# Kernel optimization log

Measured on AMD Instinct MI355X. Metric: run time of the kernel, lower is better.

The kernel has to match this reference:

```python
import jax, jax.numpy as jnp
import numpy as np

B, D, H, K = 4096, 768, 16384, 32


def setup_inputs() -> dict:
    key = jax.random.key(0)
    k1, k2, k3 = jax.random.split(key, 3)
    return {
        "x": jax.random.normal(k1, (B, D), dtype=jnp.float32),
        "W_enc": jax.random.normal(k2, (H, D), dtype=jnp.float32) * 0.02,
        "b_enc": jnp.zeros((H,), dtype=jnp.float32),
        "W_dec": jax.random.normal(k3, (D, H), dtype=jnp.float32) * 0.02,
        "b_dec": jnp.zeros((D,), dtype=jnp.float32),
        "k": K,
    }


def reference(x, W_enc, b_enc, W_dec, b_dec, k):
    # Encode: z = ReLU(x W_enc^T + b_enc)   -> [B, H]
    z = jax.nn.relu(jnp.einsum("bd,hd->bh", x, W_enc) + b_enc)
    # Top-k mask along hidden dim (k < H)
    _, topk_idx = jax.lax.top_k(z, k)                      # [B, k]
    rows = jnp.arange(z.shape[0])[:, None]                 # [B, 1]
    mask = jnp.zeros_like(z).at[rows, topk_idx].set(1.0)   # scatter ones
    z = z * mask
    # Decode: x_hat = z W_dec^T + b_dec     -> [B, D]
    x_hat = jnp.einsum("bh,dh->bd", z, W_dec) + b_dec
    return (x_hat, z)
```

## Files before the change

### kernel.cpp

```cpp
#include <hip/hip_runtime.h>

constexpr int NB = 4096;
constexpr int ND = 768;
constexpr int NH = 16384;
constexpr int NK = 32;
constexpr int CAND_MAX = 512;
#define DELTA 0.04f

typedef __bf16 bf16x8 __attribute__((ext_vector_type(8)));
typedef float  f32x4  __attribute__((ext_vector_type(4)));

constexpr size_t OFF_XBF   = 0;
constexpr size_t OFF_WENCB = OFF_XBF   + (size_t)NB * ND * 2;
constexpr size_t OFF_WDECT = OFF_WENCB + (size_t)NH * ND * 2;
constexpr size_t OFF_CIDX  = OFF_WDECT + (size_t)NH * ND * 4;
constexpr size_t OFF_CCNT  = OFF_CIDX  + (size_t)NB * CAND_MAX * 4;
constexpr size_t OFF_ZA    = OFF_CCNT  + (size_t)NB * 4;
constexpr size_t ZA_BYTES  = (size_t)NB * NH * 2;

__device__ inline unsigned short f2bf(float f) {
  unsigned u = __float_as_uint(f);
  unsigned r = u + 0x7fffu + ((u >> 16) & 1u);
  return (unsigned short)(r >> 16);
}

__device__ __forceinline__ void gld_lds16(const unsigned short* g, unsigned short* s) {
  __builtin_amdgcn_global_load_lds((const __attribute__((address_space(1))) void*)g,
                                   (__attribute__((address_space(3))) void*)s, 16, 0, 0);
}

__global__ __launch_bounds__(256) void cast_bf16_kernel(const float* __restrict__ in,
                                                        unsigned short* __restrict__ out,
                                                        int n4) {
  int stride = gridDim.x * 256;
  for (int i = blockIdx.x * 256 + threadIdx.x; i < n4; i += stride) {
    float4 v = ((const float4*)in)[i];
    unsigned long long p = (unsigned long long)f2bf(v.x)
                         | ((unsigned long long)f2bf(v.y) << 16)
                         | ((unsigned long long)f2bf(v.z) << 32)
                         | ((unsigned long long)f2bf(v.w) << 48);
    ((unsigned long long*)out)[i] = p;
  }
}

__global__ __launch_bounds__(256) void transpose_kernel(const float* __restrict__ in,
                                                        float* __restrict__ out) {
  __shared__ float tile[32][33];
  int hb = blockIdx.x * 32, db = blockIdx.y * 32;
  int tx = threadIdx.x, ty = threadIdx.y;
#pragma unroll
  for (int i = 0; i < 4; ++i)
    tile[ty + i * 8][tx] = in[(size_t)(db + ty + i * 8) * NH + hb + tx];
  __syncthreads();
#pragma unroll
  for (int i = 0; i < 4; ++i)
    out[(size_t)(hb + ty + i * 8) * ND + db + tx] = tile[tx][ty + i * 8];
}

__global__ __launch_bounds__(512) void encode_gemm_kernel(
    const unsigned short* __restrict__ Abf,
    const unsigned short* __restrict__ Bbf,
    const float* __restrict__ b_enc,
    unsigned short* __restrict__ za) {
  __shared__ __align__(16) unsigned short lds_all[3 * 16384];

  int bid = blockIdx.x;
  int xx = bid & 7;
  int jj = bid >> 3;
  int st = jj >> 4;
  int w  = jj & 15;
  int g  = st * 8 + xx;
  int bm = (g & 3) * 4 + (w & 3);
  int bn = (g >> 2) * 4 + (w >> 2);
  int m0 = bm * 256, n0 = bn * 256;

  int tid = threadIdx.x;
  int wid = tid >> 6, l = tid & 63;
  int wr = wid >> 2, wc = wid & 3;
  int lr = l & 15, lk = l >> 4;

#define STAGE_A(nbuf, ktile, t) do {                                              \
    int c_ = (t) * 512 + tid; int r_ = c_ >> 2;                                   \
    int lu_ = (c_ & 3) ^ ((r_ >> 1) & 3);                                         \
    gld_lds16(Abf + (size_t)(m0 + r_) * ND + (ktile) * 32 + lu_ * 8,              \
              lds_all + (nbuf) * 16384 + ((t) * 512 + (wid << 6)) * 8);           \
  } while (0)
#define STAGE_B(nbuf, ktile, t) do {                                              \
    int c_ = (t) * 512 + tid; int r_ = c_ >> 2;                                   \
    int lu_ = (c_ & 3) ^ ((r_ >> 1) & 3);                                         \
    gld_lds16(Bbf + (size_t)(n0 + r_) * ND + (ktile) * 32 + lu_ * 8,              \
              lds_all + (nbuf) * 16384 + 8192 + ((t) * 512 + (wid << 6)) * 8);    \
  } while (0)

  f32x4 acc[8][4] = {};

  STAGE_A(0, 0, 0); STAGE_A(0, 0, 1); STAGE_B(0, 0, 0); STAGE_B(0, 0, 1);
  STAGE_A(1, 1, 0); STAGE_A(1, 1, 1); STAGE_B(1, 1, 0); STAGE_B(1, 1, 1);
  asm volatile("s_waitcnt vmcnt(4)" ::: "memory");
  __builtin_amdgcn_s_barrier();
  __builtin_amdgcn_sched_barrier(0);

  int cur = 0;
  for (int kt = 0; kt < 24; ++kt) {
    int nx = cur + 2; if (nx >= 3) nx -= 3;
    const unsigned short* Ab = lds_all + cur * 16384;
    const unsigned short* Bb = Ab + 8192;
    bf16x8 aF[4], bF[4];

#pragma unroll
    for (int fj = 0; fj < 4; ++fj) {
      int row = wc * 64 + fj * 16 + lr;
      int pu = lk ^ ((row >> 1) & 3);
      bF[fj] = *(const bf16x8*)(Bb + row * 32 + pu * 8);
    }
#pragma unroll
    for (int fi = 0; fi < 4; ++fi) {
      int row = wr * 128 + fi * 16 + lr;
      int pu = lk ^ ((row >> 1) & 3);
      aF[fi] = *(const bf16x8*)(Ab + row * 32 + pu * 8);
    }
    if (kt < 22) { STAGE_A(nx, kt + 2, 0); STAGE_A(nx, kt + 2, 1); }
    __builtin_amdgcn_s_setprio(1);
#pragma unroll
    for (int fi = 0; fi < 4; ++fi)
#pragma unroll
      for (int fj = 0; fj < 4; ++fj)
        acc[fi][fj] = __builtin_amdgcn_mfma_f32_16x16x32_bf16(aF[fi], bF[fj], acc[fi][fj], 0, 0, 0);
    __builtin_amdgcn_s_setprio(0);

#pragma unroll
    for (int fi = 0; fi < 4; ++fi) {
      int row = wr * 128 + (4 + fi) * 16 + lr;
      int pu = lk ^ ((row >> 1) & 3);
      aF[fi] = *(const bf16x8*)(Ab + row * 32 + pu * 8);
    }
    if (kt < 22) { STAGE_B(nx, kt + 2, 0); STAGE_B(nx, kt + 2, 1); }
    __builtin_amdgcn_s_setprio(1);
#pragma unroll
    for (int fi = 0; fi < 4; ++fi)
#pragma unroll
      for (int fj = 0; fj < 4; ++fj)
        acc[4 + fi][fj] = __builtin_amdgcn_mfma_f32_16x16x32_bf16(aF[fi], bF[fj], acc[4 + fi][fj], 0, 0, 0);
    __builtin_amdgcn_s_setprio(0);

    if (kt < 23) {
      if (kt == 22) asm volatile("s_waitcnt vmcnt(0)" ::: "memory");
      else          asm volatile("s_waitcnt vmcnt(4)" ::: "memory");
      __builtin_amdgcn_s_barrier();
      __builtin_amdgcn_sched_barrier(0);
    }
    cur = (cur == 2) ? 0 : cur + 1;
  }
#undef STAGE_A
#undef STAGE_B

  __syncthreads();
  unsigned short* ep = lds_all + wid * 4096;
#pragma unroll
  for (int half = 0; half < 2; ++half) {
#pragma unroll
    for (int fj = 0; fj < 4; ++fj) {
      float bias = b_enc[n0 + wc * 64 + fj * 16 + lr];
#pragma unroll
      for (int i2 = 0; i2 < 4; ++i2) {
#pragma unroll
        for (int q = 0; q < 4; ++q) {
          int row = i2 * 16 + lk * 4 + q;
          int col = fj * 16 + lr;
          float v = fmaxf(acc[half * 4 + i2][fj][q] + bias, 0.0f);
          ep[row * 64 + (((col >> 3) ^ (row & 7)) * 8) + (col & 7)] = f2bf(v);
        }
      }
    }
    __syncthreads();
#pragma unroll
    for (int t = 0; t < 8; ++t) {
      int row = t * 8 + (l >> 3);
      int u = (l & 7) ^ (row & 7);
      int4 d = *(const int4*)&ep[row * 64 + u * 8];
      *(int4*)(za + (size_t)(m0 + wr * 128 + half * 64 + row) * NH
                    + n0 + wc * 64 + (l & 7) * 8) = d;
    }
    __syncthreads();
  }
}


__device__ __forceinline__ float bisect_thr(const uint4* v, int* wcnt, int tid) {
  unsigned lo = 0u, hi = 0x7F80u;
  for (int it = 0; it < 15; ++it) {
    unsigned mid = (lo + hi) >> 1;
    int c = 0;
#pragma unroll
    for (int i = 0; i < 8; ++i) {
      const unsigned* p = (const unsigned*)&v[i];
#pragma unroll
      for (int e = 0; e < 4; ++e) {
        unsigned u = p[e];
        c += ((u & 0xFFFFu) >= mid) ? 1 : 0;
        c += ((u >> 16) >= mid) ? 1 : 0;
      }
    }
#pragma unroll
    for (int off = 32; off; off >>= 1) c += __shfl_xor(c, off, 64);
    if ((tid & 63) == 0) wcnt[tid >> 6] = c;
    __syncthreads();
    int tot = wcnt[0] + wcnt[1] + wcnt[2] + wcnt[3];
    __syncthreads();
    if (tot >= NK) {
      lo = mid;
      if (tot <= 48) break;
    } else {
      hi = mid;
    }
  }
  float thr = __uint_as_float(lo << 16) - DELTA;
  return (thr < 1e-12f) ? 1e-12f : thr;
}

__device__ __forceinline__ void topk_wave0(const float* cv, const int* ci, int cnt,
                                           float* sv, int* si, int l) {
  float lv[8]; int lh[8];
#pragma unroll
  for (int ii = 0; ii < 8; ++ii) {
    int c = l + 64 * ii;
    if (c < cnt) { lv[ii] = cv[c]; lh[ii] = ci[c]; }
    else         { lv[ii] = -1.f;  lh[ii] = 0x7fffffff; }
  }
  for (int r = 0; r < NK; ++r) {
    float bv = -1.f; int bh = 0x7fffffff; int bl = l; int bii = 0;
#pragma unroll
    for (int ii = 0; ii < 8; ++ii)
      if (lv[ii] > bv || (lv[ii] == bv && lh[ii] < bh)) { bv = lv[ii]; bh = lh[ii]; bii = ii; }
#pragma unroll
    for (int off = 32; off; off >>= 1) {
      float ov = __shfl_xor(bv, off, 64);
      int   oh = __shfl_xor(bh, off, 64);
      int   ol = __shfl_xor(bl, off, 64);
      int   oi = __shfl_xor(bii, off, 64);
      if (ov > bv || (ov == bv && oh < bh)) { bv = ov; bh = oh; bl = ol; bii = oi; }
    }
    if (l == 0) {
      if (bv > -0.5f) { sv[r] = bv; si[r] = bh; }
      else            { sv[r] = 0.f; si[r] = -1; }
    }
#pragma unroll
    for (int ii = 0; ii < 8; ++ii)
      if (ii == bii && l == bl && bv > -0.5f) lv[ii] = -1.f;
  }
}

__global__ __launch_bounds__(256) void select_kernel(const unsigned short* __restrict__ za,
                                                     int* __restrict__ cand_idx,
                                                     int* __restrict__ cand_cnt) {
  int b = blockIdx.x, tid = threadIdx.x;
  const uint4* zrow = (const uint4*)(za + (size_t)b * NH);
  uint4 v[8];
#pragma unroll
  for (int i = 0; i < 8; ++i) v[i] = zrow[tid + 256 * i];

  __shared__ int wcnt[4];
  __shared__ int lcnt;
  float thr = bisect_thr(v, wcnt, tid);
  if (tid == 0) lcnt = 0;
  __syncthreads();
#pragma unroll
  for (int i = 0; i < 8; ++i) {
    const unsigned* p = (const unsigned*)&v[i];
#pragma unroll
    for (int e = 0; e < 4; ++e) {
      unsigned u = p[e];
      int hbase = (tid + 256 * i) * 8 + e * 2;
      float f0 = __uint_as_float((u & 0xFFFFu) << 16);
      float f1 = __uint_as_float(u & 0xFFFF0000u);
      if (f0 >= thr) { int s = atomicAdd(&lcnt, 1); if (s < CAND_MAX) cand_idx[(size_t)b * CAND_MAX + s] = hbase; }
      if (f1 >= thr) { int s = atomicAdd(&lcnt, 1); if (s < CAND_MAX) cand_idx[(size_t)b * CAND_MAX + s] = hbase + 1; }
    }
  }
  __syncthreads();
  if (tid == 0) cand_cnt[b] = (lcnt < CAND_MAX) ? lcnt : CAND_MAX;
}

__device__ __forceinline__ void finalize_core(
    int b, int tid, int wid, int l, int cnt,
    const float* __restrict__ W_enc, const float* __restrict__ b_enc,
    const float* __restrict__ WdecT, const float* __restrict__ b_dec,
    const float* xr, float* cv, const int* ci, float* sv, int* si,
    float* __restrict__ zout, float* __restrict__ xhat) {
  const float4* xr4 = (const float4*)xr;
  for (int c = wid; c < cnt; c += 4) {
    int h = ci[c];
    const float4* wrow4 = (const float4*)(W_enc + (size_t)h * ND);
    float4 s4 = make_float4(0.f, 0.f, 0.f, 0.f);
#pragma unroll
    for (int i = 0; i < 3; ++i) {
      float4 wv = wrow4[l + 64 * i];
      float4 xv = xr4[l + 64 * i];
      s4.x = fmaf(wv.x, xv.x, s4.x);
      s4.y = fmaf(wv.y, xv.y, s4.y);
      s4.z = fmaf(wv.z, xv.z, s4.z);
      s4.w = fmaf(wv.w, xv.w, s4.w);
    }
    float s = (s4.x + s4.y) + (s4.z + s4.w);
#pragma unroll
    for (int off = 32; off; off >>= 1) s += __shfl_xor(s, off, 64);
    if (l == 0) cv[c] = fmaxf(s + b_enc[h], 0.f);
  }
  __syncthreads();

  if (wid == 0) {
    topk_wave0(cv, ci, cnt, sv, si, l);
  } else {
    float4 z4 = make_float4(0.f, 0.f, 0.f, 0.f);
    float4* zr = (float4*)(zout + (size_t)b * NH);
    for (int i = tid - 64; i < NH / 4; i += 192) zr[i] = z4;
  }
  __syncthreads();

  if (tid < NK) {
    int s = si[tid];
    if (s >= 0) zout[(size_t)b * NH + s] = sv[tid];
  }

  if (tid < ND / 4) {
    float4 a = ((const float4*)b_dec)[tid];
#pragma unroll 8
    for (int j = 0; j < NK; ++j) {
      int hj = si[j]; hj = (hj < 0) ? 0 : hj;
      float vj = sv[j];
      float4 wv = ((const float4*)(WdecT + (size_t)hj * ND))[tid];
      a.x = fmaf(vj, wv.x, a.x);
      a.y = fmaf(vj, wv.y, a.y);
      a.z = fmaf(vj, wv.z, a.z);
      a.w = fmaf(vj, wv.w, a.w);
    }
    ((float4*)(xhat + (size_t)b * ND))[tid] = a;
  }
}

__global__ __launch_bounds__(256) void finalize_kernel(
    const float* __restrict__ x, const float* __restrict__ W_enc,
    const float* __restrict__ b_enc,
    const int* __restrict__ cand_idx, const int* __restrict__ cand_cnt,
    const float* __restrict__ WdecT, const float* __restrict__ b_dec,
    float* __restrict__ zout, float* __restrict__ xhat) {
  int b = blockIdx.x, tid = threadIdx.x;
  int wid = tid >> 6, l = tid & 63;
  __shared__ __align__(16) float xr[ND];
  __shared__ float cv[CAND_MAX];
  __shared__ int   ci[CAND_MAX];
  __shared__ float sv[NK];
  __shared__ int   si[NK];

  int cnt = cand_cnt[b];
  const float4* xrow = (const float4*)(x + (size_t)b * ND);
  for (int i = tid; i < ND / 4; i += 256) ((float4*)xr)[i] = xrow[i];
  for (int c = tid; c < cnt; c += 256) ci[c] = cand_idx[(size_t)b * CAND_MAX + c];
  __syncthreads();
  finalize_core(b, tid, wid, l, cnt, W_enc, b_enc, WdecT, b_dec,
                xr, cv, ci, sv, si, zout, xhat);
}

__global__ __launch_bounds__(256) void fused_finalize_kernel(
    const unsigned short* __restrict__ za,
    const float* __restrict__ x, const float* __restrict__ W_enc,
    const float* __restrict__ b_enc,
    const float* __restrict__ WdecT, const float* __restrict__ b_dec,
    float* __restrict__ zout, float* __restrict__ xhat) {
  int b = blockIdx.x, tid = threadIdx.x;
  int wid = tid >> 6, l = tid & 63;
  __shared__ __align__(16) float xr[ND];
  __shared__ float cv[CAND_MAX];
  __shared__ int   ci[CAND_MAX];
  __shared__ float sv[NK];
  __shared__ int   si[NK];
  __shared__ int   wcnt[4];
  __shared__ int   lcnt;

  const uint4* zrow = (const uint4*)(za + (size_t)b * NH);
  uint4 v[8];
#pragma unroll
  for (int i = 0; i < 8; ++i) v[i] = zrow[tid + 256 * i];
  const float4* xrow = (const float4*)(x + (size_t)b * ND);
  for (int i = tid; i < ND / 4; i += 256) ((float4*)xr)[i] = xrow[i];

  float thr = bisect_thr(v, wcnt, tid);
  if (tid == 0) lcnt = 0;
  __syncthreads();
#pragma unroll
  for (int i = 0; i < 8; ++i) {
    const unsigned* p = (const unsigned*)&v[i];
#pragma unroll
    for (int e = 0; e < 4; ++e) {
      unsigned u = p[e];
      int hbase = (tid + 256 * i) * 8 + e * 2;
      float f0 = __uint_as_float((u & 0xFFFFu) << 16);
      float f1 = __uint_as_float(u & 0xFFFF0000u);
      if (f0 >= thr) { int s = atomicAdd(&lcnt, 1); if (s < CAND_MAX) ci[s] = hbase; }
      if (f1 >= thr) { int s = atomicAdd(&lcnt, 1); if (s < CAND_MAX) ci[s] = hbase + 1; }
    }
  }
  __syncthreads();
  int cnt = (lcnt < CAND_MAX) ? lcnt : CAND_MAX;

  finalize_core(b, tid, wid, l, cnt, W_enc, b_enc, WdecT, b_dec,
                xr, cv, ci, sv, si, zout, xhat);
}

extern "C" void kernel_launch(void* const* d_in, const int* in_sizes, int n_in,
                              void* d_out, int out_size, void* d_ws, size_t ws_size,
                              hipStream_t stream) {
  const float* x     = (const float*)d_in[0];
  const float* W_enc = (const float*)d_in[1];
  const float* b_enc = (const float*)d_in[2];
  const float* W_dec = (const float*)d_in[3];
  const float* b_dec = (const float*)d_in[4];

  float* xhat = (float*)d_out;
  float* zout = (float*)d_out + (size_t)NB * ND;

  char* ws = (char*)d_ws;
  unsigned short* x_bf    = (unsigned short*)(ws + OFF_XBF);
  unsigned short* wenc_bf = (unsigned short*)(ws + OFF_WENCB);
  float*          wdecT   = (float*)(ws + OFF_WDECT);
  int*            cidx    = (int*)(ws + OFF_CIDX);
  int*            ccnt    = (int*)(ws + OFF_CCNT);

  bool fused = ws_size >= OFF_ZA + ZA_BYTES;
  unsigned short* za = fused ? (unsigned short*)(ws + OFF_ZA)
                             : (unsigned short*)zout;

  cast_bf16_kernel<<<1024, 256, 0, stream>>>(x, x_bf, NB * ND / 4);
  cast_bf16_kernel<<<2048, 256, 0, stream>>>(W_enc, wenc_bf, NH * ND / 4);
  transpose_kernel<<<dim3(NH / 32, ND / 32), dim3(32, 8), 0, stream>>>(W_dec, wdecT);
  encode_gemm_kernel<<<(NB / 256) * (NH / 256), 512, 0, stream>>>(x_bf, wenc_bf, b_enc, za);
  if (fused) {
    fused_finalize_kernel<<<NB, 256, 0, stream>>>(za, x, W_enc, b_enc, wdecT, b_dec, zout, xhat);
  } else {
    select_kernel<<<NB, 256, 0, stream>>>(za, cidx, ccnt);
    finalize_kernel<<<NB, 256, 0, stream>>>(x, W_enc, b_enc, cidx, ccnt, wdecT, b_dec, zout, xhat);
  }
}
```

Measured before the change: 358.3 us.

## Merge prep kernels and overlap z-output zeroing with encode GEMM

Combines the two bf16 cast kernels and the W_dec transpose into one prep kernel, removing two launches and their tail gaps. On the fused path, the 256 MB z output is now zeroed inside the encode GEMM's k-loop using nontemporal stores, so these writes overlap MFMA compute instead of running in the finalize kernel. Finalize then writes only the top-k entries. The risk is that the extra stores compete with the GEMM for memory bandwidth and issue slots.

```diff
diff --git a/kernel.cpp b/kernel.cpp
--- a/kernel.cpp
+++ b/kernel.cpp
@@ -29,39 +29,52 @@
                                    (__attribute__((address_space(3))) void*)s, 16, 0, 0);
 }
 
-__global__ __launch_bounds__(256) void cast_bf16_kernel(const float* __restrict__ in,
-                                                        unsigned short* __restrict__ out,
-                                                        int n4) {
-  int stride = gridDim.x * 256;
-  for (int i = blockIdx.x * 256 + threadIdx.x; i < n4; i += stride) {
-    float4 v = ((const float4*)in)[i];
-    unsigned long long p = (unsigned long long)f2bf(v.x)
-                         | ((unsigned long long)f2bf(v.y) << 16)
-                         | ((unsigned long long)f2bf(v.z) << 32)
-                         | ((unsigned long long)f2bf(v.w) << 48);
-    ((unsigned long long*)out)[i] = p;
-  }
-}
-
-__global__ __launch_bounds__(256) void transpose_kernel(const float* __restrict__ in,
-                                                        float* __restrict__ out) {
-  __shared__ float tile[32][33];
-  int hb = blockIdx.x * 32, db = blockIdx.y * 32;
-  int tx = threadIdx.x, ty = threadIdx.y;
-#pragma unroll
-  for (int i = 0; i < 4; ++i)
-    tile[ty + i * 8][tx] = in[(size_t)(db + ty + i * 8) * NH + hb + tx];
-  __syncthreads();
-#pragma unroll
-  for (int i = 0; i < 4; ++i)
-    out[(size_t)(hb + ty + i * 8) * ND + db + tx] = tile[tx][ty + i * 8];
+__global__ __launch_bounds__(256) void prep_kernel(
+    const float* __restrict__ x, unsigned short* __restrict__ x_bf,
+    const float* __restrict__ W_enc, unsigned short* __restrict__ wenc_bf,
+    const float* __restrict__ W_dec, float* __restrict__ wdecT) {
+  int b = blockIdx.x, tid = threadIdx.x;
+  if (b < 1024) {
+    int n4 = NB * ND / 4, stride = 1024 * 256;
+    for (int i = b * 256 + tid; i < n4; i += stride) {
+      float4 v = ((const float4*)x)[i];
+      unsigned long long p = (unsigned long long)f2bf(v.x)
+                           | ((unsigned long long)f2bf(v.y) << 16)
+                           | ((unsigned long long)f2bf(v.z) << 32)
+                           | ((unsigned long long)f2bf(v.w) << 48);
+      ((unsigned long long*)x_bf)[i] = p;
+    }
+  } else if (b < 3072) {
+    int n4 = NH * ND / 4, stride = 2048 * 256;
+    for (int i = (b - 1024) * 256 + tid; i < n4; i += stride) {
+      float4 v = ((const float4*)W_enc)[i];
+      unsigned long long p = (unsigned long long)f2bf(v.x)
+                           | ((unsigned long long)f2bf(v.y) << 16)
+                           | ((unsigned long long)f2bf(v.z) << 32)
+                           | ((unsigned long long)f2bf(v.w) << 48);
+      ((unsigned long long*)wenc_bf)[i] = p;
+    }
+  } else {
+    __shared__ float tile[32][33];
+    int tb = b - 3072;
+    int hb = (tb & 511) * 32, db = (tb >> 9) * 32;
+    int tx = tid & 31, ty = tid >> 5;
+#pragma unroll
+    for (int i = 0; i < 4; ++i)
+      tile[ty + i * 8][tx] = W_dec[(size_t)(db + ty + i * 8) * NH + hb + tx];
+    __syncthreads();
+#pragma unroll
+    for (int i = 0; i < 4; ++i)
+      wdecT[(size_t)(hb + ty + i * 8) * ND + db + tx] = tile[tx][ty + i * 8];
+  }
 }
 
 __global__ __launch_bounds__(512) void encode_gemm_kernel(
     const unsigned short* __restrict__ Abf,
     const unsigned short* __restrict__ Bbf,
     const float* __restrict__ b_enc,
-    unsigned short* __restrict__ za) {
+    unsigned short* __restrict__ za,
+    float* __restrict__ zzero) {
   __shared__ __align__(16) unsigned short lds_all[3 * 16384];
 
   int bid = blockIdx.x;
@@ -120,6 +133,15 @@
       aF[fi] = *(const bf16x8*)(Ab + row * 32 + pu * 8);
     }
     if (kt < 22) { STAGE_A(nx, kt + 2, 0); STAGE_A(nx, kt + 2, 1); }
+    if (zzero && kt < 16) {
+      f32x4 zz = {0.f, 0.f, 0.f, 0.f};
+#pragma unroll
+      for (int z2 = 0; z2 < 2; ++z2) {
+        int idx = (kt * 2 + z2) * 512 + tid;
+        int row = idx >> 6, col = idx & 63;
+        __builtin_nontemporal_store(zz, (f32x4*)(zzero + (size_t)(m0 + row) * NH + n0) + col);
+      }
+    }
     __builtin_amdgcn_s_setprio(1);
 #pragma unroll
     for (int fi = 0; fi < 4; ++fi)
@@ -286,7 +308,7 @@
     const float* __restrict__ W_enc, const float* __restrict__ b_enc,
     const float* __restrict__ WdecT, const float* __restrict__ b_dec,
     const float* xr, float* cv, const int* ci, float* sv, int* si,
-    float* __restrict__ zout, float* __restrict__ xhat) {
+    float* __restrict__ zout, float* __restrict__ xhat, bool zero_z) {
   const float4* xr4 = (const float4*)xr;
   for (int c = wid; c < cnt; c += 4) {
     int h = ci[c];
@@ -310,7 +332,7 @@
 
   if (wid == 0) {
     topk_wave0(cv, ci, cnt, sv, si, l);
-  } else {
+  } else if (zero_z) {
     float4 z4 = make_float4(0.f, 0.f, 0.f, 0.f);
     float4* zr = (float4*)(zout + (size_t)b * NH);
     for (int i = tid - 64; i < NH / 4; i += 192) zr[i] = z4;
@@ -358,7 +380,7 @@
   for (int c = tid; c < cnt; c += 256) ci[c] = cand_idx[(size_t)b * CAND_MAX + c];
   __syncthreads();
   finalize_core(b, tid, wid, l, cnt, W_enc, b_enc, WdecT, b_dec,
-                xr, cv, ci, sv, si, zout, xhat);
+                xr, cv, ci, sv, si, zout, xhat, true);
 }
 
 __global__ __launch_bounds__(256) void fused_finalize_kernel(
@@ -404,7 +426,7 @@
   int cnt = (lcnt < CAND_MAX) ? lcnt : CAND_MAX;
 
   finalize_core(b, tid, wid, l, cnt, W_enc, b_enc, WdecT, b_dec,
-                xr, cv, ci, sv, si, zout, xhat);
+                xr, cv, ci, sv, si, zout, xhat, false);
 }
 
 extern "C" void kernel_launch(void* const* d_in, const int* in_sizes, int n_in,
@@ -430,10 +452,9 @@
   unsigned short* za = fused ? (unsigned short*)(ws + OFF_ZA)
                              : (unsigned short*)zout;
 
-  cast_bf16_kernel<<<1024, 256, 0, stream>>>(x, x_bf, NB * ND / 4);
-  cast_bf16_kernel<<<2048, 256, 0, stream>>>(W_enc, wenc_bf, NH * ND / 4);
-  transpose_kernel<<<dim3(NH / 32, ND / 32), dim3(32, 8), 0, stream>>>(W_dec, wdecT);
-  encode_gemm_kernel<<<(NB / 256) * (NH / 256), 512, 0, stream>>>(x_bf, wenc_bf, b_enc, za);
+  prep_kernel<<<15360, 256, 0, stream>>>(x, x_bf, W_enc, wenc_bf, W_dec, wdecT);
+  encode_gemm_kernel<<<(NB / 256) * (NH / 256), 512, 0, stream>>>(
+      x_bf, wenc_bf, b_enc, za, fused ? zout : nullptr);
   if (fused) {
     fused_finalize_kernel<<<NB, 256, 0, stream>>>(za, x, W_enc, b_enc, wdecT, b_dec, zout, xhat);
   } else {
```

Measured after the change: 385.7 us. 1.08x slower.
